# Optimization experiments

Hardware: AMD Instinct MI355X
Metric: run time of the kernel (lower is better)

Reference implementation:

```python
import jax, jax.numpy as jnp
import numpy as np

N = 100000   # nodes
E = 1600000  # edges
D_IN, D_H, D_OUT = 128, 256, 128
EPS = 1e-5


def _linear_params(key, fan_in, fan_out):
    lim = 1.0 / np.sqrt(fan_in)
    kw, kb = jax.random.split(key)
    W = jax.random.uniform(kw, (fan_in, fan_out), minval=-lim, maxval=lim, dtype=jnp.float32)
    b = jax.random.uniform(kb, (fan_out,), minval=-lim, maxval=lim, dtype=jnp.float32)
    return W, b


def setup_inputs() -> dict:
    key = jax.random.key(0)
    ks = jax.random.split(key, 8)
    W1, b1 = _linear_params(ks[0], D_IN, D_H)
    W2, b2 = _linear_params(ks[1], D_H, D_H)
    W3, b3 = _linear_params(ks[2], D_H, D_OUT)
    return {
        'feat': jax.random.normal(ks[3], (N, D_IN), dtype=jnp.float32),
        'W1': W1, 'b1': b1, 'g1': jnp.ones(D_H, jnp.float32), 'be1': jnp.zeros(D_H, jnp.float32), 'a1': jnp.full((1,), 0.25, jnp.float32),
        'W2': W2, 'b2': b2, 'g2': jnp.ones(D_H, jnp.float32), 'be2': jnp.zeros(D_H, jnp.float32), 'a2': jnp.full((1,), 0.25, jnp.float32),
        'W3': W3, 'b3': b3,
        'src': jax.random.randint(ks[4], (E,), 0, N, dtype=jnp.int32),
        'dst': jax.random.randint(ks[5], (E,), 0, N, dtype=jnp.int32),
    }


def _layer_norm(x, g, b):
    mu = jnp.mean(x, axis=-1, keepdims=True)
    var = jnp.mean((x - mu) ** 2, axis=-1, keepdims=True)
    return g * (x - mu) / jnp.sqrt(var + EPS) + b


def _prelu(x, a):
    return jnp.where(x >= 0, x, a * x)


def reference(feat, W1, b1, g1, be1, a1, W2, b2, g2, be2, a2, W3, b3, src, dst):
    ones = jnp.ones((E,), jnp.float32)
    # out-degree (of src nodes) and in-degree (of dst nodes), clamped to >= 1
    deg_out = jnp.maximum(jax.ops.segment_sum(ones, src, num_segments=N), 1.0) ** -0.5  # [N]
    deg_in = jnp.maximum(jax.ops.segment_sum(ones, dst, num_segments=N), 1.0) ** -0.5   # [N]

    def conv(h, W, b, g=None, be=None, a=None):
        x = h * deg_out[:, None]                                   # src-side degree norm
        agg = jax.ops.segment_sum(x[src], dst, num_segments=N)     # sparse sum aggregation
        r = (agg @ W + b) * deg_in[:, None]                        # linear + dst-side norm
        if g is not None:
            r = _prelu(_layer_norm(r, g, be), a)
        return r

    h = conv(feat, W1, b1, g1, be1, a1)
    h = conv(h, W2, b2, g2, be2, a2)
    h = conv(h, W3, b3)  # last layer: encoding=False -> no norm, no activation
    return h
```

## Files before the change

kernel.cpp:

```cpp
#include <hip/hip_runtime.h>
#include <cstdint>
#include <cstddef>

static constexpr int NN = 100000;
static constexpr int NE = 1600000;
static constexpr int NP = 100096;

static constexpr int NBUCK  = 391;
static constexpr int BCAP   = 5120;
static constexpr int NBUCKD = 782;
static constexpr int BCAPD  = 2816;
static constexpr int SCAP   = 128;
static constexpr int PBLK   = 200;
static constexpr int EPB    = 8000;

typedef __attribute__((ext_vector_type(8))) short short8;
typedef __attribute__((ext_vector_type(8))) unsigned short ushort8;
typedef __attribute__((ext_vector_type(4))) float f32x4;

__device__ inline ushort bf16_rtn(float x) {
    uint32_t u = __float_as_uint(x);
    uint32_t r = u + 0x7fffu + ((u >> 16) & 1u);
    return (ushort)(r >> 16);
}
__device__ inline float bf16_to_f(ushort u) {
    return __uint_as_float((uint32_t)u << 16);
}

__global__ __launch_bounds__(256) void k_init_cur(int* __restrict__ curA) {
    int b = blockIdx.x * 256 + threadIdx.x;
    if (b < NBUCK) curA[b] = b * BCAP;
}

__global__ __launch_bounds__(256) void k_partA(const int* __restrict__ src, const int* __restrict__ dst,
                                               int* __restrict__ curA, int* __restrict__ pairA) {
    __shared__ int hs[NBUCK];
    int e0 = blockIdx.x * EPB;
    for (int i = threadIdx.x; i < NBUCK; i += 256) hs[i] = 0;
    __syncthreads();
    for (int e = e0 + (int)threadIdx.x; e < e0 + EPB; e += 256)
        atomicAdd(&hs[src[e] >> 8], 1);
    __syncthreads();
    for (int i = threadIdx.x; i < NBUCK; i += 256) {
        int c = hs[i];
        hs[i] = c ? atomicAdd(&curA[i], c) : 0;
    }
    __syncthreads();
    for (int e = e0 + (int)threadIdx.x; e < e0 + EPB; e += 256) {
        int s = src[e], d = dst[e];
        int p = atomicAdd(&hs[s >> 8], 1);
        pairA[p] = (d << 8) | (s & 255);
    }
}

__global__ __launch_bounds__(256) void k_degout(const int* __restrict__ curA, const int* __restrict__ pairA,
                                                float* __restrict__ deg_out_inv) {
    __shared__ int h[256];
    int b = blockIdx.x;
    int p0 = b * BCAP;
    int n = curA[b] - p0;
    h[threadIdx.x] = 0;
    __syncthreads();
    for (int i = threadIdx.x; i < n; i += 256)
        atomicAdd(&h[pairA[p0 + i] & 255], 1);
    __syncthreads();
    int node = b * 256 + (int)threadIdx.x;
    if (node < NN)
        deg_out_inv[node] = rsqrtf(fmaxf((float)h[threadIdx.x], 1.0f));
}

__global__ __launch_bounds__(256) void k_countB(const int* __restrict__ curA, const int* __restrict__ pairA,
                                                int* __restrict__ cntB) {
    __shared__ int h[NBUCKD];
    int s = blockIdx.x;
    int p0 = s * BCAP;
    int n = curA[s] - p0;
    for (int i = threadIdx.x; i < NBUCKD; i += 256) h[i] = 0;
    __syncthreads();
    for (int i = threadIdx.x; i < n; i += 256)
        atomicAdd(&h[pairA[p0 + i] >> 15], 1);
    __syncthreads();
    for (int i = threadIdx.x; i < NBUCKD; i += 256)
        cntB[s * NBUCKD + i] = h[i];
}

__global__ __launch_bounds__(512) void k_scanB(const int* __restrict__ cntB, int* __restrict__ offB,
                                               int* __restrict__ fillB) {
    __shared__ int sd[512];
    int b = blockIdx.x;
    int t = threadIdx.x;
    int v = (t < NBUCK) ? cntB[t * NBUCKD + b] : 0;
    sd[t] = v;
    __syncthreads();
    #pragma unroll
    for (int off = 1; off < 512; off <<= 1) {
        int x = (t >= off) ? sd[t - off] : 0;
        __syncthreads();
        sd[t] += x;
        __syncthreads();
    }
    if (t < NBUCK) offB[t * NBUCKD + b] = b * BCAPD + sd[t] - v;
    if (t == NBUCK - 1) fillB[b] = sd[t];
}

__global__ __launch_bounds__(256) void k_placeB(const int* __restrict__ curA, const int* __restrict__ pairA,
                                                const int* __restrict__ offB, int* __restrict__ pairB) {
    __shared__ int cur[NBUCKD];
    int s = blockIdx.x;
    int p0 = s * BCAP;
    int n = curA[s] - p0;
    for (int i = threadIdx.x; i < NBUCKD; i += 256) cur[i] = offB[s * NBUCKD + i];
    __syncthreads();
    int sbase = s << 8;
    for (int i = threadIdx.x; i < n; i += 256) {
        int pk = pairA[p0 + i];
        int d = pk >> 8;
        int sfull = sbase | (pk & 255);
        int pos = atomicAdd(&cur[d >> 7], 1);
        pairB[pos] = (sfull << 7) | (d & 127);
    }
}

__global__ __launch_bounds__(256) void k_deg_in(const int* __restrict__ fillB, const int* __restrict__ pairB,
                                                float* __restrict__ deg_in_inv) {
    __shared__ int h[128];
    int b = blockIdx.x;
    int p0 = b * BCAPD;
    int n = fillB[b];
    if (threadIdx.x < 128) h[threadIdx.x] = 0;
    __syncthreads();
    for (int i = threadIdx.x; i < n; i += 256)
        atomicAdd(&h[pairB[p0 + i] & 127], 1);
    __syncthreads();
    if (threadIdx.x < 128) {
        int node = b * 128 + (int)threadIdx.x;
        deg_in_inv[node] = rsqrtf(fmaxf((float)h[threadIdx.x], 1.0f));
    }
}

__global__ __launch_bounds__(512) void k_split32(const int* __restrict__ fillB, const int* __restrict__ pairB,
                                                 int* __restrict__ pairB2, int* __restrict__ fillS) {
    __shared__ int se[BCAPD];
    int b = blockIdx.x;
    int n = fillB[b];
    const int* ep = pairB + (size_t)b * BCAPD;
    for (int i = threadIdx.x; i < n; i += 512) se[i] = ep[i];
    __syncthreads();
    int w = threadIdx.x >> 6;
    int l = threadIdx.x & 63;
    for (int r = 0; r < 4; ++r) {
        int h = w + 8 * r;
        int* op = pairB2 + (size_t)(b * 32 + h) * SCAP;
        int cnt = 0;
        for (int i0 = 0; i0 < n; i0 += 64) {
            int idx = i0 + l;
            int pk = (idx < n) ? se[idx] : 0;
            bool match = (idx < n) && ((pk & 31) == h);
            unsigned long long mask = __ballot(match);
            if (match) {
                int pos = __popcll(mask & ((1ull << l) - 1ull));
                op[cnt + pos] = pk;
            }
            cnt += __popcll(mask);
        }
        if (l == 0) fillS[b * 32 + h] = cnt;
    }
}

__global__ __launch_bounds__(256) void k_cvt(const float* __restrict__ feat,
                                             const float* __restrict__ deg_out_inv,
                                             ushort* __restrict__ out) {
    int idx = blockIdx.x * 256 + threadIdx.x;
    if (idx >= NN * 32) return;
    float4 v = *(const float4*)(feat + (size_t)idx * 4);
    float w = deg_out_inv[idx >> 5];
    ushort4 o;
    o.x = bf16_rtn(v.x * w);
    o.y = bf16_rtn(v.y * w);
    o.z = bf16_rtn(v.z * w);
    o.w = bf16_rtn(v.w * w);
    *(ushort4*)(out + (size_t)idx * 4) = o;
}

template <int XSTRIDE, int COLOFF, bool FINAL>
__global__ __launch_bounds__(1024) void k_agg_push3(const int* __restrict__ pairB2, const int* __restrict__ fillS,
                                                    const ushort* __restrict__ x,
                                                    const float* __restrict__ bias,
                                                    const float* __restrict__ deg_in_inv,
                                                    ushort* __restrict__ out_b, float* __restrict__ out_f) {
    __shared__ float lacc[128 * 128];
    int b = blockIdx.x;
    for (int i = threadIdx.x; i < 4096; i += 1024)
        *(float4*)&lacc[i * 4] = (float4){0.f, 0.f, 0.f, 0.f};
    __syncthreads();
    int h = threadIdx.x >> 5;
    int l5 = threadIdx.x & 31;
    int sb = b * 32 + h;
    int m = fillS[sb];
    const int* ep = pairB2 + (size_t)sb * SCAP;
    const ushort* xb = x + COLOFF + l5 * 4;
    for (int i0 = 0; i0 < m; i0 += 4) {
        int4 pks = *(const int4*)(ep + i0);
        int pk[4] = {pks.x, pks.y, pks.z, pks.w};
        ushort4 v[4];
        float wt[4];
        #pragma unroll
        for (int j = 0; j < 4; ++j) {
            bool ok = (i0 + j < m);
            wt[j] = ok ? 1.0f : 0.0f;
            pk[j] = ok ? pk[j] : pk[0];
            v[j] = *(const ushort4*)(xb + (size_t)(pk[j] >> 7) * XSTRIDE);
        }
        #pragma unroll
        for (int j = 0; j < 4; ++j) {
            int a = (pk[j] & 127) * 128 + l5 * 4;
            float4 c = *(float4*)&lacc[a];
            c.x += wt[j] * bf16_to_f(v[j].x);
            c.y += wt[j] * bf16_to_f(v[j].y);
            c.z += wt[j] * bf16_to_f(v[j].z);
            c.w += wt[j] * bf16_to_f(v[j].w);
            *(float4*)&lacc[a] = c;
        }
    }
    __syncthreads();
    int row = threadIdx.x >> 3;
    int cg = threadIdx.x & 7;
    int node = b * 128 + row;
    const float* lp = &lacc[row * 128 + cg * 16];
    if constexpr (FINAL) {
        if (node < NN) {
            float dv = deg_in_inv[node];
            float* op = out_f + (size_t)node * 128 + cg * 16;
            #pragma unroll
            for (int gq = 0; gq < 4; ++gq) {
                float4 c = *(const float4*)(lp + gq * 4);
                float4 bv = *(const float4*)(bias + cg * 16 + gq * 4);
                float4 o;
                o.x = (c.x + bv.x) * dv;
                o.y = (c.y + bv.y) * dv;
                o.z = (c.z + bv.z) * dv;
                o.w = (c.w + bv.w) * dv;
                *(float4*)(op + gq * 4) = o;
            }
        }
    } else {
        ushort8 u0, u1;
        #pragma unroll
        for (int k = 0; k < 8; ++k) {
            u0[k] = bf16_rtn(lp[k]);
            u1[k] = bf16_rtn(lp[8 + k]);
        }
        ushort* op = out_b + (size_t)node * XSTRIDE + COLOFF + cg * 16;
        *(ushort8*)op = u0;
        *(ushort8*)(op + 8) = u1;
    }
}

template <int K, int M>
__device__ inline void packW_dev(const float* __restrict__ W, ushort* __restrict__ out, int blk) {
    constexpr int NT = M / 16, KC = K / 32;
    constexpr int WTOT = KC * NT * 512;
    int idx = blk * 256 + (int)threadIdx.x;
    int lane = idx & 63;
    int tile = idx >> 6;
    int nt = tile % NT, kc = tile / NT;
    int col = nt * 16 + (lane & 15);
    int kbase = kc * 32 + (lane >> 4) * 8;
    size_t o = (size_t)tile * 512 + lane * 8;
    #pragma unroll
    for (int j = 0; j < 8; ++j) {
        float w = W[(size_t)(kbase + j) * M + col];
        uint32_t u = __float_as_uint(w);
        uint32_t hu = u & 0xffff0000u;
        float lf = w - __uint_as_float(hu);
        out[o + j] = (ushort)(u >> 16);
        out[o + WTOT + j] = (ushort)(__float_as_uint(lf) >> 16);
    }
}

__global__ __launch_bounds__(256) void k_packAll(const float* __restrict__ W1, ushort* __restrict__ o1,
                                                 const float* __restrict__ W2, ushort* __restrict__ o2,
                                                 const float* __restrict__ W3, ushort* __restrict__ o3) {
    int b = blockIdx.x;
    if (b < 16) packW_dev<128, 256>(W1, o1, b);
    else if (b < 48) packW_dev<256, 256>(W2, o2, b - 16);
    else packW_dev<256, 128>(W3, o3, b - 48);
}

template <int K, int M, int MODE>
__global__ __launch_bounds__(256) void k_gemm_mfma(const ushort* __restrict__ A,
                                                   const ushort* __restrict__ Wp,
                                                   const float* __restrict__ bias,
                                                   const float* __restrict__ deg_in_inv,
                                                   const float* __restrict__ deg_out_inv,
                                                   const float* __restrict__ g,
                                                   const float* __restrict__ be,
                                                   const float* __restrict__ a,
                                                   ushort* __restrict__ out) {
    constexpr int NT = M / 16;
    constexpr int KC = K / 32;
    constexpr int WTOT = KC * NT * 512;
    constexpr int COLW = M / 64;
    constexpr int ROWW = 4 / COLW;
    constexpr int BROWS = 64 * ROWW;
    constexpr int LROW = M + 8;
    constexpr int NRF = BROWS / 16;
    constexpr int RFW = NRF / 4;
    __shared__ ushort sbuf[BROWS * LROW];
    __shared__ float sredS[4][64];
    __shared__ float sredQ[4][64];
    __shared__ float smu[64];
    __shared__ float srs[64];
    static_assert(BROWS * LROW >= 2 * NRF * 512, "staging dbuf must fit in sbuf");

    int lane = threadIdx.x & 63;
    int wave = threadIdx.x >> 6;
    int cw = wave % COLW;
    int rw = wave / COLW;
    int m = lane & 15;
    int quad = lane >> 4;
    int rowb = blockIdx.x * BROWS + rw * 64;

    f32x4 acc[4][4];
    #pragma unroll
    for (int rf = 0; rf < 4; ++rf)
        #pragma unroll
        for (int ct = 0; ct < 4; ++ct) acc[rf][ct] = (f32x4){0.f, 0.f, 0.f, 0.f};

    const size_t arow0 = (size_t)blockIdx.x * BROWS;
    auto stage = [&](int kc, int buf) {
        #pragma unroll
        for (int s = 0; s < RFW; ++s) {
            int rf = wave * RFW + s;
            const ushort* gsrc = A + (arow0 + rf * 16 + m) * K + kc * 32 + quad * 8;
            ushort* ldst = sbuf + (size_t)(buf * NRF + rf) * 512;
            __builtin_amdgcn_global_load_lds(
                (const __attribute__((address_space(1))) unsigned int*)gsrc,
                (__attribute__((address_space(3))) unsigned int*)ldst, 16, 0, 0);
        }
    };
    stage(0, 0);
    __syncthreads();
    for (int kc = 0; kc < KC; ++kc) {
        if (kc + 1 < KC) stage(kc + 1, (kc + 1) & 1);
        const ushort* ab = sbuf + (size_t)((kc & 1) * NRF + rw * 4) * 512 + lane * 8;
        short8 av[4];
        #pragma unroll
        for (int rf = 0; rf < 4; ++rf)
            av[rf] = *(const short8*)(ab + rf * 512);
        const ushort* wb0 = Wp + ((size_t)kc * NT + cw * 4) * 512 + lane * 8;
        #pragma unroll
        for (int ct = 0; ct < 4; ++ct) {
            short8 bh = *(const short8*)(wb0 + ct * 512);
            short8 bl = *(const short8*)(wb0 + WTOT + ct * 512);
            #pragma unroll
            for (int rf = 0; rf < 4; ++rf) {
                acc[rf][ct] = __builtin_amdgcn_mfma_f32_16x16x32_bf16(av[rf], bh, acc[rf][ct], 0, 0, 0);
                acc[rf][ct] = __builtin_amdgcn_mfma_f32_16x16x32_bf16(av[rf], bl, acc[rf][ct], 0, 0, 0);
            }
        }
        __syncthreads();
    }
    if constexpr (MODE == 1) {
        float bia[4];
        #pragma unroll
        for (int ct = 0; ct < 4; ++ct) bia[ct] = bias[cw * 64 + ct * 16 + m];
        float din[4][4], fold[4][4];
        #pragma unroll
        for (int rf = 0; rf < 4; ++rf)
            #pragma unroll
            for (int r = 0; r < 4; ++r) {
                int row = rowb + rf * 16 + quad * 4 + r;
                din[rf][r] = deg_in_inv[row];
                fold[rf][r] = deg_out_inv[row];
            }
        float s[4][4], q[4][4];
        #pragma unroll
        for (int rf = 0; rf < 4; ++rf)
            #pragma unroll
            for (int r = 0; r < 4; ++r) { s[rf][r] = 0.f; q[rf][r] = 0.f; }
        #pragma unroll
        for (int rf = 0; rf < 4; ++rf)
            #pragma unroll
            for (int ct = 0; ct < 4; ++ct)
                #pragma unroll
                for (int r = 0; r < 4; ++r) {
                    float v = (acc[rf][ct][r] + bia[ct]) * din[rf][r];
                    acc[rf][ct][r] = v;
                    s[rf][r] += v;
                    q[rf][r] += v * v;
                }
        #pragma unroll
        for (int w = 1; w < 16; w <<= 1)
            #pragma unroll
            for (int rf = 0; rf < 4; ++rf)
                #pragma unroll
                for (int r = 0; r < 4; ++r) {
                    s[rf][r] += __shfl_xor(s[rf][r], w);
                    q[rf][r] += __shfl_xor(q[rf][r], w);
                }
        if (m == 0) {
            #pragma unroll
            for (int rf = 0; rf < 4; ++rf)
                #pragma unroll
                for (int r = 0; r < 4; ++r) {
                    int rl = rf * 16 + quad * 4 + r;
                    sredS[wave][rl] = s[rf][r];
                    sredQ[wave][rl] = q[rf][r];
                }
        }
        __syncthreads();
        if (threadIdx.x < 64) {
            int rl = threadIdx.x;
            float st = sredS[0][rl] + sredS[1][rl] + sredS[2][rl] + sredS[3][rl];
            float qt = sredQ[0][rl] + sredQ[1][rl] + sredQ[2][rl] + sredQ[3][rl];
            float mu = st * (1.0f / M);
            float var = qt * (1.0f / M) - mu * mu;
            smu[rl] = mu;
            srs[rl] = rsqrtf(var + 1e-5f);
        }
        __syncthreads();
        float alpha = a[0];
        float gv[4], bev[4];
        #pragma unroll
        for (int ct = 0; ct < 4; ++ct) {
            gv[ct] = g[cw * 64 + ct * 16 + m];
            bev[ct] = be[cw * 64 + ct * 16 + m];
        }
        #pragma unroll
        for (int rf = 0; rf < 4; ++rf)
            #pragma unroll
            for (int r = 0; r < 4; ++r) {
                int rl = rf * 16 + quad * 4 + r;
                float mu = smu[rl];
                float rs = srs[rl];
                float fo = fold[rf][r];
                #pragma unroll
                for (int ct = 0; ct < 4; ++ct) {
                    float v = gv[ct] * (acc[rf][ct][r] - mu) * rs + bev[ct];
                    v = (v >= 0.0f) ? v : alpha * v;
                    v *= fo;
                    sbuf[rl * LROW + cw * 64 + ct * 16 + m] = bf16_rtn(v);
                }
            }
    } else {
        #pragma unroll
        for (int rf = 0; rf < 4; ++rf)
            #pragma unroll
            for (int ct = 0; ct < 4; ++ct)
                #pragma unroll
                for (int r = 0; r < 4; ++r)
                    sbuf[(rw * 64 + rf * 16 + quad * 4 + r) * LROW + cw * 64 + ct * 16 + m] =
                        bf16_rtn(acc[rf][ct][r]);
    }
    __syncthreads();
    constexpr int CNT = BROWS * M / 256;
    int trow = ((int)threadIdx.x * CNT) / M;
    int tcol = ((int)threadIdx.x * CNT) % M;
    const ushort* rsrc = sbuf + trow * LROW + tcol;
    ushort* gdst = out + (size_t)(blockIdx.x * BROWS + trow) * M + tcol;
    #pragma unroll
    for (int j = 0; j < CNT / 8; ++j) {
        ushort8 v = *(const ushort8*)(rsrc + j * 8);
        *(ushort8*)(gdst + j * 8) = v;
    }
}

extern "C" void kernel_launch(void* const* d_in, const int* in_sizes, int n_in,
                              void* d_out, int out_size, void* d_ws, size_t ws_size,
                              hipStream_t stream) {
    const float* feat = (const float*)d_in[0];
    const float* W1 = (const float*)d_in[1];
    const float* b1 = (const float*)d_in[2];
    const float* g1 = (const float*)d_in[3];
    const float* be1 = (const float*)d_in[4];
    const float* a1 = (const float*)d_in[5];
    const float* W2 = (const float*)d_in[6];
    const float* b2 = (const float*)d_in[7];
    const float* g2 = (const float*)d_in[8];
    const float* be2 = (const float*)d_in[9];
    const float* a2 = (const float*)d_in[10];
    const float* W3 = (const float*)d_in[11];
    const float* b3 = (const float*)d_in[12];
    const int* src = (const int*)d_in[13];
    const int* dst = (const int*)d_in[14];

    char* ws = (char*)d_ws;
    size_t off = 0;
    auto alloc = [&](size_t bytes) -> void* {
        off = (off + 511) & ~(size_t)511;
        void* p = ws + off;
        off += bytes;
        return p;
    };
    int* curA = (int*)alloc((size_t)NBUCK * 4);
    float* deg_out_inv = (float*)alloc((size_t)NP * 4);
    float* deg_in_inv = (float*)alloc((size_t)NP * 4);
    int* pairA = (int*)alloc((size_t)NBUCK * BCAP * 4);
    int* pairB = (int*)alloc((size_t)NBUCKD * BCAPD * 4);
    int* pairB2 = (int*)alloc((size_t)NBUCKD * 32 * SCAP * 4);
    int* fillS = (int*)alloc((size_t)NBUCKD * 32 * 4);
    int* cntB = (int*)alloc((size_t)NBUCK * NBUCKD * 4);
    int* offB = (int*)alloc((size_t)NBUCK * NBUCKD * 4);
    int* fillB = (int*)alloc((size_t)NBUCKD * 4);
    ushort* Wp1 = (ushort*)alloc((size_t)2 * 4 * 16 * 512 * 2);
    ushort* Wp2 = (ushort*)alloc((size_t)2 * 8 * 16 * 512 * 2);
    ushort* Wp3 = (ushort*)alloc((size_t)2 * 8 * 8 * 512 * 2);
    ushort* featb = (ushort*)alloc((size_t)NP * 128 * 2);
    ushort* aggb  = (ushort*)alloc((size_t)NP * 256 * 2);
    ushort* hb    = (ushort*)alloc((size_t)NP * 256 * 2);
    ushort* yb    = (ushort*)alloc((size_t)NP * 128 * 2);
    (void)ws_size; (void)in_sizes; (void)n_in; (void)out_size;

    k_init_cur<<<2, 256, 0, stream>>>(curA);
    k_partA<<<PBLK, 256, 0, stream>>>(src, dst, curA, pairA);
    k_degout<<<NBUCK, 256, 0, stream>>>(curA, pairA, deg_out_inv);
    k_countB<<<NBUCK, 256, 0, stream>>>(curA, pairA, cntB);
    k_scanB<<<NBUCKD, 512, 0, stream>>>(cntB, offB, fillB);
    k_placeB<<<NBUCK, 256, 0, stream>>>(curA, pairA, offB, pairB);
    k_deg_in<<<NBUCKD, 256, 0, stream>>>(fillB, pairB, deg_in_inv);
    k_split32<<<NBUCKD, 512, 0, stream>>>(fillB, pairB, pairB2, fillS);

    k_packAll<<<64, 256, 0, stream>>>(W1, Wp1, W2, Wp2, W3, Wp3);
    k_cvt<<<(NN * 32 + 255) / 256, 256, 0, stream>>>(feat, deg_out_inv, featb);

    k_agg_push3<128, 0, false><<<NBUCKD, 1024, 0, stream>>>(pairB2, fillS, featb, nullptr, nullptr, aggb, nullptr);
    k_gemm_mfma<128, 256, 1><<<NP / 64, 256, 0, stream>>>(aggb, Wp1, b1, deg_in_inv, deg_out_inv, g1, be1, a1, hb);

    k_agg_push3<256, 0, false><<<NBUCKD, 1024, 0, stream>>>(pairB2, fillS, hb, nullptr, nullptr, aggb, nullptr);
    k_agg_push3<256, 128, false><<<NBUCKD, 1024, 0, stream>>>(pairB2, fillS, hb, nullptr, nullptr, aggb, nullptr);
    k_gemm_mfma<256, 256, 1><<<NP / 64, 256, 0, stream>>>(aggb, Wp2, b2, deg_in_inv, deg_out_inv, g2, be2, a2, hb);

    k_gemm_mfma<256, 128, 0><<<NP / 128, 256, 0, stream>>>(hb, Wp3, nullptr, nullptr, nullptr, nullptr, nullptr, nullptr, yb);
    k_agg_push3<128, 0, true><<<NBUCKD, 1024, 0, stream>>>(pairB2, fillS, yb, b3, deg_in_inv, nullptr, (float*)d_out);
}
```

Before: 638.4 us.

## Accumulate edge aggregation in registers instead of shared-memory tile

The aggregation kernel no longer keeps a 128x128 fp32 shared-memory accumulator. Each 32-lane group now keeps four float4 accumulators in registers, one per destination row it owns, and picks the row from bits 5-6 of the packed edge key using predicated FMAs. This drops the LDS zero-fill, the LDS read-modify-write per edge and both block barriers, and frees 64KB of LDS per block so more blocks can fit on a CU. The price is four times more FMAs per edge, and the inner loop is unrolled by two instead of four, which leaves fewer gathers in flight. It also relies on each sub-bucket holding only destinations whose low 5 bits match its group index.

New measurement: 707.9 us. +10.9%, slower.

```diff
diff --git a/kernel.cpp b/kernel.cpp
--- a/kernel.cpp
+++ b/kernel.cpp
@@ -16,6 +16,7 @@
 
 typedef __attribute__((ext_vector_type(8))) short short8;
 typedef __attribute__((ext_vector_type(8))) unsigned short ushort8;
+typedef __attribute__((ext_vector_type(4))) unsigned short ushort4v;
 typedef __attribute__((ext_vector_type(4))) float f32x4;
 
 __device__ inline ushort bf16_rtn(float x) {
@@ -183,76 +184,65 @@
 }
 
 template <int XSTRIDE, int COLOFF, bool FINAL>
-__global__ __launch_bounds__(1024) void k_agg_push3(const int* __restrict__ pairB2, const int* __restrict__ fillS,
+__global__ __launch_bounds__(1024) void k_agg_push5(const int* __restrict__ pairB2,
+                                                    const int* __restrict__ fillS,
                                                     const ushort* __restrict__ x,
                                                     const float* __restrict__ bias,
                                                     const float* __restrict__ deg_in_inv,
                                                     ushort* __restrict__ out_b, float* __restrict__ out_f) {
-    __shared__ float lacc[128 * 128];
     int b = blockIdx.x;
-    for (int i = threadIdx.x; i < 4096; i += 1024)
-        *(float4*)&lacc[i * 4] = (float4){0.f, 0.f, 0.f, 0.f};
-    __syncthreads();
-    int h = threadIdx.x >> 5;
-    int l5 = threadIdx.x & 31;
+    int h = (int)threadIdx.x >> 5;
+    int l5 = (int)threadIdx.x & 31;
     int sb = b * 32 + h;
     int m = fillS[sb];
     const int* ep = pairB2 + (size_t)sb * SCAP;
     const ushort* xb = x + COLOFF + l5 * 4;
-    for (int i0 = 0; i0 < m; i0 += 4) {
-        int4 pks = *(const int4*)(ep + i0);
-        int pk[4] = {pks.x, pks.y, pks.z, pks.w};
-        ushort4 v[4];
-        float wt[4];
-        #pragma unroll
-        for (int j = 0; j < 4; ++j) {
-            bool ok = (i0 + j < m);
-            wt[j] = ok ? 1.0f : 0.0f;
-            pk[j] = ok ? pk[j] : pk[0];
-            v[j] = *(const ushort4*)(xb + (size_t)(pk[j] >> 7) * XSTRIDE);
-        }
-        #pragma unroll
-        for (int j = 0; j < 4; ++j) {
-            int a = (pk[j] & 127) * 128 + l5 * 4;
-            float4 c = *(float4*)&lacc[a];
-            c.x += wt[j] * bf16_to_f(v[j].x);
-            c.y += wt[j] * bf16_to_f(v[j].y);
-            c.z += wt[j] * bf16_to_f(v[j].z);
-            c.w += wt[j] * bf16_to_f(v[j].w);
-            *(float4*)&lacc[a] = c;
-        }
-    }
-    __syncthreads();
-    int row = threadIdx.x >> 3;
-    int cg = threadIdx.x & 7;
-    int node = b * 128 + row;
-    const float* lp = &lacc[row * 128 + cg * 16];
+    f32x4 acc[4];
+    #pragma unroll
+    for (int r = 0; r < 4; ++r) acc[r] = (f32x4){0.f, 0.f, 0.f, 0.f};
+    for (int i = 0; i < m; i += 2) {
+        int pk0 = ep[i];
+        int i1 = (i + 1 < m) ? (i + 1) : i;
+        int pk1 = ep[i1];
+        float wt1 = (i + 1 < m) ? 1.0f : 0.0f;
+        ushort4v v0 = *(const ushort4v*)(xb + (size_t)(pk0 >> 7) * XSTRIDE);
+        ushort4v v1 = *(const ushort4v*)(xb + (size_t)(pk1 >> 7) * XSTRIDE);
+        int s0 = (pk0 >> 5) & 3;
+        int s1 = (pk1 >> 5) & 3;
+        #pragma unroll
+        for (int r = 0; r < 4; ++r) {
+            float w0 = (s0 == r) ? 1.0f : 0.0f;
+            float w1 = (s1 == r) ? wt1 : 0.0f;
+            #pragma unroll
+            for (int k = 0; k < 4; ++k)
+                acc[r][k] = fmaf(w0, bf16_to_f(v0[k]),
+                             fmaf(w1, bf16_to_f(v1[k]), acc[r][k]));
+        }
+    }
     if constexpr (FINAL) {
-        if (node < NN) {
-            float dv = deg_in_inv[node];
-            float* op = out_f + (size_t)node * 128 + cg * 16;
-            #pragma unroll
-            for (int gq = 0; gq < 4; ++gq) {
-                float4 c = *(const float4*)(lp + gq * 4);
-                float4 bv = *(const float4*)(bias + cg * 16 + gq * 4);
+        float4 bv = *(const float4*)(bias + COLOFF + l5 * 4);
+        #pragma unroll
+        for (int r = 0; r < 4; ++r) {
+            int node = b * 128 + h + 32 * r;
+            if (node < NN) {
+                float dv = deg_in_inv[node];
                 float4 o;
-                o.x = (c.x + bv.x) * dv;
-                o.y = (c.y + bv.y) * dv;
-                o.z = (c.z + bv.z) * dv;
-                o.w = (c.w + bv.w) * dv;
-                *(float4*)(op + gq * 4) = o;
+                o.x = (acc[r][0] + bv.x) * dv;
+                o.y = (acc[r][1] + bv.y) * dv;
+                o.z = (acc[r][2] + bv.z) * dv;
+                o.w = (acc[r][3] + bv.w) * dv;
+                *(float4*)(out_f + (size_t)node * 128 + COLOFF + l5 * 4) = o;
             }
         }
     } else {
-        ushort8 u0, u1;
-        #pragma unroll
-        for (int k = 0; k < 8; ++k) {
-            u0[k] = bf16_rtn(lp[k]);
-            u1[k] = bf16_rtn(lp[8 + k]);
-        }
-        ushort* op = out_b + (size_t)node * XSTRIDE + COLOFF + cg * 16;
-        *(ushort8*)op = u0;
-        *(ushort8*)(op + 8) = u1;
+        #pragma unroll
+        for (int r = 0; r < 4; ++r) {
+            int node = b * 128 + h + 32 * r;
+            ushort4v u;
+            #pragma unroll
+            for (int k = 0; k < 4; ++k) u[k] = bf16_rtn(acc[r][k]);
+            *(ushort4v*)(out_b + (size_t)node * XSTRIDE + COLOFF + l5 * 4) = u;
+        }
     }
 }
 
@@ -524,13 +514,13 @@
     k_packAll<<<64, 256, 0, stream>>>(W1, Wp1, W2, Wp2, W3, Wp3);
     k_cvt<<<(NN * 32 + 255) / 256, 256, 0, stream>>>(feat, deg_out_inv, featb);
 
-    k_agg_push3<128, 0, false><<<NBUCKD, 1024, 0, stream>>>(pairB2, fillS, featb, nullptr, nullptr, aggb, nullptr);
+    k_agg_push5<128, 0, false><<<NBUCKD, 1024, 0, stream>>>(pairB2, fillS, featb, nullptr, nullptr, aggb, nullptr);
     k_gemm_mfma<128, 256, 1><<<NP / 64, 256, 0, stream>>>(aggb, Wp1, b1, deg_in_inv, deg_out_inv, g1, be1, a1, hb);
 
-    k_agg_push3<256, 0, false><<<NBUCKD, 1024, 0, stream>>>(pairB2, fillS, hb, nullptr, nullptr, aggb, nullptr);
-    k_agg_push3<256, 128, false><<<NBUCKD, 1024, 0, stream>>>(pairB2, fillS, hb, nullptr, nullptr, aggb, nullptr);
+    k_agg_push5<256, 0, false><<<NBUCKD, 1024, 0, stream>>>(pairB2, fillS, hb, nullptr, nullptr, aggb, nullptr);
+    k_agg_push5<256, 128, false><<<NBUCKD, 1024, 0, stream>>>(pairB2, fillS, hb, nullptr, nullptr, aggb, nullptr);
     k_gemm_mfma<256, 256, 1><<<NP / 64, 256, 0, stream>>>(aggb, Wp2, b2, deg_in_inv, deg_out_inv, g2, be2, a2, hb);
 
     k_gemm_mfma<256, 128, 0><<<NP / 128, 256, 0, stream>>>(hb, Wp3, nullptr, nullptr, nullptr, nullptr, nullptr, nullptr, yb);
-    k_agg_push3<128, 0, true><<<NBUCKD, 1024, 0, stream>>>(pairB2, fillS, yb, b3, deg_in_inv, nullptr, (float*)d_out);
-}
+    k_agg_push5<128, 0, true><<<NBUCKD, 1024, 0, stream>>>(pairB2, fillS, yb, b3, deg_in_inv, nullptr, (float*)d_out);
+}
```

## Halve destination buckets to 64 nodes, double LDS accumulators, fuse in-degree into split

Applied to the files above, without the earlier changes.

Destination buckets shrink from 128 to 64 nodes, which doubles the block count of the aggregation kernels. Each block's LDS accumulator is split into two copies, alternating by edge parity, to cut read-modify-write conflicts between lanes. The in-degree histogram kernel is folded into the split kernel to save a pass and a launch. The aim is better occupancy and parallelism for the scatter aggregation. The risk is that smaller per-sub-bucket capacities (SCAP 96, BCAPD 1536) could overflow on skewed degree distributions.

Measured after the change: 651.9 us. 1.02x slower.

```diff
diff --git a/kernel.cpp b/kernel.cpp
--- a/kernel.cpp
+++ b/kernel.cpp
@@ -8,14 +8,15 @@
 
 static constexpr int NBUCK  = 391;
 static constexpr int BCAP   = 5120;
-static constexpr int NBUCKD = 782;
-static constexpr int BCAPD  = 2816;
-static constexpr int SCAP   = 128;
+static constexpr int NBUCKD = 1564;
+static constexpr int BCAPD  = 1536;
+static constexpr int SCAP   = 96;
 static constexpr int PBLK   = 200;
 static constexpr int EPB    = 8000;
 
 typedef __attribute__((ext_vector_type(8))) short short8;
 typedef __attribute__((ext_vector_type(8))) unsigned short ushort8;
+typedef __attribute__((ext_vector_type(4))) unsigned short ushort4v;
 typedef __attribute__((ext_vector_type(4))) float f32x4;
 
 __device__ inline ushort bf16_rtn(float x) {
@@ -78,7 +79,7 @@
     for (int i = threadIdx.x; i < NBUCKD; i += 256) h[i] = 0;
     __syncthreads();
     for (int i = threadIdx.x; i < n; i += 256)
-        atomicAdd(&h[pairA[p0 + i] >> 15], 1);
+        atomicAdd(&h[pairA[p0 + i] >> 14], 1);
     __syncthreads();
     for (int i = threadIdx.x; i < NBUCKD; i += 256)
         cntB[s * NBUCKD + i] = h[i];
@@ -116,42 +117,37 @@
         int pk = pairA[p0 + i];
         int d = pk >> 8;
         int sfull = sbase | (pk & 255);
-        int pos = atomicAdd(&cur[d >> 7], 1);
-        pairB[pos] = (sfull << 7) | (d & 127);
-    }
-}
-
-__global__ __launch_bounds__(256) void k_deg_in(const int* __restrict__ fillB, const int* __restrict__ pairB,
-                                                float* __restrict__ deg_in_inv) {
-    __shared__ int h[128];
-    int b = blockIdx.x;
-    int p0 = b * BCAPD;
-    int n = fillB[b];
-    if (threadIdx.x < 128) h[threadIdx.x] = 0;
-    __syncthreads();
-    for (int i = threadIdx.x; i < n; i += 256)
-        atomicAdd(&h[pairB[p0 + i] & 127], 1);
-    __syncthreads();
-    if (threadIdx.x < 128) {
-        int node = b * 128 + (int)threadIdx.x;
-        deg_in_inv[node] = rsqrtf(fmaxf((float)h[threadIdx.x], 1.0f));
-    }
-}
-
-__global__ __launch_bounds__(512) void k_split32(const int* __restrict__ fillB, const int* __restrict__ pairB,
-                                                 int* __restrict__ pairB2, int* __restrict__ fillS) {
+        int pos = atomicAdd(&cur[d >> 6], 1);
+        pairB[pos] = (sfull << 6) | (d & 63);
+    }
+}
+
+__global__ __launch_bounds__(512) void k_split32d(const int* __restrict__ fillB, const int* __restrict__ pairB,
+                                                  int* __restrict__ pairB2, int* __restrict__ fillS,
+                                                  float* __restrict__ deg_in_inv) {
     __shared__ int se[BCAPD];
+    __shared__ int cnt[64];
     int b = blockIdx.x;
     int n = fillB[b];
     const int* ep = pairB + (size_t)b * BCAPD;
-    for (int i = threadIdx.x; i < n; i += 512) se[i] = ep[i];
-    __syncthreads();
+    if (threadIdx.x < 64) cnt[threadIdx.x] = 0;
+    __syncthreads();
+    for (int i = threadIdx.x; i < n; i += 512) {
+        int pk = ep[i];
+        se[i] = pk;
+        atomicAdd(&cnt[pk & 63], 1);
+    }
+    __syncthreads();
+    if (threadIdx.x < 64) {
+        int node = b * 64 + (int)threadIdx.x;
+        deg_in_inv[node] = rsqrtf(fmaxf((float)cnt[threadIdx.x], 1.0f));
+    }
     int w = threadIdx.x >> 6;
     int l = threadIdx.x & 63;
     for (int r = 0; r < 4; ++r) {
         int h = w + 8 * r;
         int* op = pairB2 + (size_t)(b * 32 + h) * SCAP;
-        int cnt = 0;
+        int c2 = 0;
         for (int i0 = 0; i0 < n; i0 += 64) {
             int idx = i0 + l;
             int pk = (idx < n) ? se[idx] : 0;
@@ -159,11 +155,11 @@
             unsigned long long mask = __ballot(match);
             if (match) {
                 int pos = __popcll(mask & ((1ull << l) - 1ull));
-                op[cnt + pos] = pk;
+                op[c2 + pos] = pk;
             }
-            cnt += __popcll(mask);
-        }
-        if (l == 0) fillS[b * 32 + h] = cnt;
+            c2 += __popcll(mask);
+        }
+        if (l == 0) fillS[b * 32 + h] = c2;
     }
 }
 
@@ -183,76 +179,72 @@
 }
 
 template <int XSTRIDE, int COLOFF, bool FINAL>
-__global__ __launch_bounds__(1024) void k_agg_push3(const int* __restrict__ pairB2, const int* __restrict__ fillS,
+__global__ __launch_bounds__(1024) void k_agg_push7(const int* __restrict__ pairB2,
+                                                    const int* __restrict__ fillS,
                                                     const ushort* __restrict__ x,
                                                     const float* __restrict__ bias,
                                                     const float* __restrict__ deg_in_inv,
                                                     ushort* __restrict__ out_b, float* __restrict__ out_f) {
-    __shared__ float lacc[128 * 128];
+    __shared__ float lacc[2 * 64 * 128];
     int b = blockIdx.x;
     for (int i = threadIdx.x; i < 4096; i += 1024)
         *(float4*)&lacc[i * 4] = (float4){0.f, 0.f, 0.f, 0.f};
     __syncthreads();
-    int h = threadIdx.x >> 5;
-    int l5 = threadIdx.x & 31;
-    int sb = b * 32 + h;
-    int m = fillS[sb];
-    const int* ep = pairB2 + (size_t)sb * SCAP;
+    int h = (int)threadIdx.x >> 5;
+    int l5 = (int)threadIdx.x & 31;
+    int m = fillS[b * 32 + h];
+    const int* ep = pairB2 + (size_t)(b * 32 + h) * SCAP;
     const ushort* xb = x + COLOFF + l5 * 4;
-    for (int i0 = 0; i0 < m; i0 += 4) {
-        int4 pks = *(const int4*)(ep + i0);
+    for (int i = 0; i < m; i += 4) {
+        int4 pks = *(const int4*)(ep + i);
         int pk[4] = {pks.x, pks.y, pks.z, pks.w};
-        ushort4 v[4];
+        ushort4v v[4];
         float wt[4];
         #pragma unroll
         for (int j = 0; j < 4; ++j) {
-            bool ok = (i0 + j < m);
+            bool ok = (i + j) < m;
             wt[j] = ok ? 1.0f : 0.0f;
             pk[j] = ok ? pk[j] : pk[0];
-            v[j] = *(const ushort4*)(xb + (size_t)(pk[j] >> 7) * XSTRIDE);
+            v[j] = *(const ushort4v*)(xb + (size_t)(pk[j] >> 6) * XSTRIDE);
         }
         #pragma unroll
         for (int j = 0; j < 4; ++j) {
-            int a = (pk[j] & 127) * 128 + l5 * 4;
+            int a = ((j & 1) << 13) + (pk[j] & 63) * 128 + l5 * 4;
             float4 c = *(float4*)&lacc[a];
-            c.x += wt[j] * bf16_to_f(v[j].x);
-            c.y += wt[j] * bf16_to_f(v[j].y);
-            c.z += wt[j] * bf16_to_f(v[j].z);
-            c.w += wt[j] * bf16_to_f(v[j].w);
+            c.x = fmaf(wt[j], bf16_to_f(v[j][0]), c.x);
+            c.y = fmaf(wt[j], bf16_to_f(v[j][1]), c.y);
+            c.z = fmaf(wt[j], bf16_to_f(v[j][2]), c.z);
+            c.w = fmaf(wt[j], bf16_to_f(v[j][3]), c.w);
             *(float4*)&lacc[a] = c;
         }
     }
     __syncthreads();
-    int row = threadIdx.x >> 3;
-    int cg = threadIdx.x & 7;
-    int node = b * 128 + row;
-    const float* lp = &lacc[row * 128 + cg * 16];
+    int row = (int)threadIdx.x >> 4;
+    int cg = (int)threadIdx.x & 15;
+    int node = b * 64 + row;
+    const float* p0 = &lacc[row * 128 + cg * 8];
+    const float* p1 = p0 + 8192;
     if constexpr (FINAL) {
         if (node < NN) {
             float dv = deg_in_inv[node];
-            float* op = out_f + (size_t)node * 128 + cg * 16;
-            #pragma unroll
-            for (int gq = 0; gq < 4; ++gq) {
-                float4 c = *(const float4*)(lp + gq * 4);
-                float4 bv = *(const float4*)(bias + cg * 16 + gq * 4);
+            #pragma unroll
+            for (int q = 0; q < 2; ++q) {
+                float4 c0 = *(const float4*)(p0 + q * 4);
+                float4 c1 = *(const float4*)(p1 + q * 4);
+                float4 bv = *(const float4*)(bias + cg * 8 + q * 4);
                 float4 o;
-                o.x = (c.x + bv.x) * dv;
-                o.y = (c.y + bv.y) * dv;
-                o.z = (c.z + bv.z) * dv;
-                o.w = (c.w + bv.w) * dv;
-                *(float4*)(op + gq * 4) = o;
+                o.x = (c0.x + c1.x + bv.x) * dv;
+                o.y = (c0.y + c1.y + bv.y) * dv;
+                o.z = (c0.z + c1.z + bv.z) * dv;
+                o.w = (c0.w + c1.w + bv.w) * dv;
+                *(float4*)(out_f + (size_t)node * 128 + cg * 8 + q * 4) = o;
             }
         }
     } else {
-        ushort8 u0, u1;
-        #pragma unroll
-        for (int k = 0; k < 8; ++k) {
-            u0[k] = bf16_rtn(lp[k]);
-            u1[k] = bf16_rtn(lp[8 + k]);
-        }
-        ushort* op = out_b + (size_t)node * XSTRIDE + COLOFF + cg * 16;
-        *(ushort8*)op = u0;
-        *(ushort8*)(op + 8) = u1;
+        ushort8 u;
+        #pragma unroll
+        for (int k = 0; k < 8; ++k) u[k] = bf16_rtn(p0[k] + p1[k]);
+        *(ushort8*)(out_b + (size_t)node * XSTRIDE + COLOFF + cg * 8) = u;
     }
 }
 
@@ -518,19 +510,18 @@
     k_countB<<<NBUCK, 256, 0, stream>>>(curA, pairA, cntB);
     k_scanB<<<NBUCKD, 512, 0, stream>>>(cntB, offB, fillB);
     k_placeB<<<NBUCK, 256, 0, stream>>>(curA, pairA, offB, pairB);
-    k_deg_in<<<NBUCKD, 256, 0, stream>>>(fillB, pairB, deg_in_inv);
-    k_split32<<<NBUCKD, 512, 0, stream>>>(fillB, pairB, pairB2, fillS);
+    k_split32d<<<NBUCKD, 512, 0, stream>>>(fillB, pairB, pairB2, fillS, deg_in_inv);
 
     k_packAll<<<64, 256, 0, stream>>>(W1, Wp1, W2, Wp2, W3, Wp3);
     k_cvt<<<(NN * 32 + 255) / 256, 256, 0, stream>>>(feat, deg_out_inv, featb);
 
-    k_agg_push3<128, 0, false><<<NBUCKD, 1024, 0, stream>>>(pairB2, fillS, featb, nullptr, nullptr, aggb, nullptr);
+    k_agg_push7<128, 0, false><<<NBUCKD, 1024, 0, stream>>>(pairB2, fillS, featb, nullptr, nullptr, aggb, nullptr);
     k_gemm_mfma<128, 256, 1><<<NP / 64, 256, 0, stream>>>(aggb, Wp1, b1, deg_in_inv, deg_out_inv, g1, be1, a1, hb);
 
-    k_agg_push3<256, 0, false><<<NBUCKD, 1024, 0, stream>>>(pairB2, fillS, hb, nullptr, nullptr, aggb, nullptr);
-    k_agg_push3<256, 128, false><<<NBUCKD, 1024, 0, stream>>>(pairB2, fillS, hb, nullptr, nullptr, aggb, nullptr);
+    k_agg_push7<256, 0, false><<<NBUCKD, 1024, 0, stream>>>(pairB2, fillS, hb, nullptr, nullptr, aggb, nullptr);
+    k_agg_push7<256, 128, false><<<NBUCKD, 1024, 0, stream>>>(pairB2, fillS, hb, nullptr, nullptr, aggb, nullptr);
     k_gemm_mfma<256, 256, 1><<<NP / 64, 256, 0, stream>>>(aggb, Wp2, b2, deg_in_inv, deg_out_inv, g2, be2, a2, hb);
 
     k_gemm_mfma<256, 128, 0><<<NP / 128, 256, 0, stream>>>(hb, Wp3, nullptr, nullptr, nullptr, nullptr, nullptr, nullptr, yb);
-    k_agg_push3<128, 0, true><<<NBUCKD, 1024, 0, stream>>>(pairB2, fillS, yb, b3, deg_in_inv, nullptr, (float*)d_out);
-}
+    k_agg_push7<128, 0, true><<<NBUCKD, 1024, 0, stream>>>(pairB2, fillS, yb, b3, deg_in_inv, nullptr, (float*)d_out);
+}
```
